# Performance work log

Measured on AMD Instinct MI355X. Metric: run time of the kernel, lower is better.

## Reference

```python
import jax, jax.numpy as jnp
import numpy as np

DIM = 2048
DIM_HEAD = 64
HEADS = 16
KV_HEADS = 2
GROUPS = HEADS // KV_HEADS  # 8
B, N = 2, 2048


def setup_inputs() -> dict:
    key = jax.random.key(0)
    k1, k2, k3, k4 = jax.random.split(key, 4)
    s = 0.02
    tokens = jax.random.normal(k1, (B, N, DIM), dtype=jnp.float32)
    context_mask = jnp.ones((B, N), dtype=bool)
    Wq = jax.random.normal(k2, (DIM, HEADS * DIM_HEAD), dtype=jnp.float32) * s
    Wkv = jax.random.normal(k3, (DIM, 2 * KV_HEADS * DIM_HEAD), dtype=jnp.float32) * s
    Wo = jax.random.normal(k4, (HEADS * DIM_HEAD, DIM), dtype=jnp.float32) * s
    return {"tokens": tokens, "context_mask": context_mask, "Wq": Wq, "Wkv": Wkv, "Wo": Wo}


def reference(tokens, context_mask, Wq, Wkv, Wo):
    b, n, _ = tokens.shape
    scale = DIM_HEAD ** -0.5
    # projections (self-attention: context = tokens)
    q = tokens @ Wq                     # [b, n, heads*dh]
    kv = tokens @ Wkv                   # [b, n, 2*kv_heads*dh]
    k, v = jnp.split(kv, 2, axis=-1)    # each [b, n, kv_heads*dh]
    # split heads: q -> [b, g, h, n, d]; k,v -> [b, h, n, d]
    q = q.reshape(b, n, GROUPS, KV_HEADS, DIM_HEAD).transpose(0, 2, 3, 1, 4)
    k = k.reshape(b, n, KV_HEADS, DIM_HEAD).transpose(0, 2, 1, 3)
    v = v.reshape(b, n, KV_HEADS, DIM_HEAD).transpose(0, 2, 1, 3)
    q = q * scale
    sim = jnp.einsum('bghid,bhjd->bghij', q, k)
    neg = -jnp.finfo(sim.dtype).max
    sim = jnp.where(context_mask[:, None, None, None, :], sim, neg)
    attn = jax.nn.softmax(sim, axis=-1)
    out = jnp.einsum('bghij,bhjd->bghid', attn, v)
    out = out.transpose(0, 3, 1, 2, 4).reshape(b, n, GROUPS * KV_HEADS * DIM_HEAD)
    return out @ Wo
```

## Files before the change

kernel.cpp:

```cpp
#include <hip/hip_runtime.h>


typedef float  f32x4   __attribute__((ext_vector_type(4)));
typedef float  f32x16  __attribute__((ext_vector_type(16)));
typedef unsigned u32x4 __attribute__((ext_vector_type(4)));
typedef __bf16 bf16x8  __attribute__((ext_vector_type(8)));
typedef __bf16 bf16x4  __attribute__((ext_vector_type(4)));

typedef f32x4  f32x4a  __attribute__((may_alias));
typedef u32x4  u32x4a  __attribute__((may_alias));
typedef bf16x8 bf16x8a __attribute__((may_alias));
typedef bf16x4 bf16x4a __attribute__((may_alias));

#define MFMA16(A, B, C) __builtin_amdgcn_mfma_f32_16x16x32_bf16(A, B, C, 0, 0, 0)
#define MFMA32(A, B, C) __builtin_amdgcn_mfma_f32_32x32x16_bf16(A, B, C, 0, 0, 0)

__device__ __forceinline__ void gload16(const void* g, void* l) {
  __builtin_amdgcn_global_load_lds(
      (const __attribute__((address_space(1))) unsigned int*)g,
      (__attribute__((address_space(3))) unsigned int*)l, 16, 0, 0);
}

__device__ __forceinline__ unsigned pack2(float a, float b) {
  union { __bf16 h[2]; unsigned u; } x;
  x.h[0] = (__bf16)a; x.h[1] = (__bf16)b;
  return x.u;
}

__device__ __forceinline__ float exp2_raw(float x) {
  float y;
  asm("v_exp_f32 %0, %1" : "=v"(y) : "v"(x));
  return y;
}

__global__ __launch_bounds__(256) void cvt_tokens(const float* __restrict__ in,
                                                  __bf16* __restrict__ out) {
  size_t idx = (size_t)blockIdx.x * 256 + threadIdx.x;
  f32x4 a = ((const f32x4a*)in)[idx * 2];
  f32x4 c = ((const f32x4a*)in)[idx * 2 + 1];
  bf16x8 v;
#pragma unroll
  for (int r = 0; r < 4; r++) { v[r] = (__bf16)a[r]; v[4 + r] = (__bf16)c[r]; }
  *(bf16x8a*)(out + idx * 8) = v;
}

__global__ __launch_bounds__(256) void transpose_all(const float* __restrict__ Wq,
                                                     const float* __restrict__ Wkv,
                                                     const float* __restrict__ Wo,
                                                     __bf16* __restrict__ WT,
                                                     __bf16* __restrict__ WoT,
                                                     float qscale) {
  const int z = blockIdx.z;
  const float* in;
  __bf16* out;
  int K, N, rowoff;
  float scale;
  if (z == 0)      { in = Wq;  out = WT;  K = 2048; N = 1024; scale = qscale; rowoff = 0; }
  else if (z == 1) { in = Wkv; out = WT;  K = 2048; N = 256;  scale = 1.f;    rowoff = 1024; }
  else             { in = Wo;  out = WoT; K = 1024; N = 2048; scale = 1.f;    rowoff = 0; }
  const int n0 = blockIdx.x * 32, k0 = blockIdx.y * 32;
  if (n0 >= N || k0 >= K) return;
  __shared__ float tile[32][33];
  const int tx = threadIdx.x, ty = threadIdx.y;
#pragma unroll
  for (int i2 = 0; i2 < 32; i2 += 8)
    tile[ty + i2][tx] = in[(size_t)(k0 + ty + i2) * N + n0 + tx];
  __syncthreads();
#pragma unroll
  for (int i2 = 0; i2 < 32; i2 += 8)
    out[(size_t)(rowoff + n0 + ty + i2) * K + k0 + tx] =
        (__bf16)(tile[tx][ty + i2] * scale);
}

__global__ __launch_bounds__(256) void build_kvpack(const __bf16* __restrict__ qkv,
                                                    __bf16* __restrict__ kv) {
  __shared__ __bf16 vt[32][64];
  const int tid = threadIdx.x;
  const int t = blockIdx.x, bh = blockIdx.y;
  const int b = bh >> 1, h = bh & 1;
  const size_t srow = (size_t)b * 2048 + (size_t)t * 32;
  __bf16* dst = kv + ((size_t)bh * 64 + t) * 4096;
  {
    int c = tid >> 5, j = tid & 31;
    bf16x8 v = *(const bf16x8a*)(qkv + (srow + j) * 1280 + 1024 + h * 64 + c * 8);
    *(bf16x8a*)(dst + tid * 8) = v;
  }
  {
    int j = tid >> 3, d8 = tid & 7;
    bf16x8 v = *(const bf16x8a*)(qkv + (srow + j) * 1280 + 1152 + h * 64 + d8 * 8);
    *(bf16x8a*)(&vt[j][d8 * 8]) = v;
  }
  __syncthreads();
  {
    int jc = tid >> 6, d = tid & 63;
    bf16x8 w;
#pragma unroll
    for (int e = 0; e < 8; e++) w[e] = vt[jc * 8 + e][d];
    *(bf16x8a*)(dst + 2048 + tid * 8) = w;
  }
}

template <int KTOT, int LDA, int LDC, bool CF32, int NX>
__global__ __launch_bounds__(512, 4) void gemm_w8(const __bf16* __restrict__ A,
                                                  const __bf16* __restrict__ Bt,
                                                  void* __restrict__ Cp) {
  __shared__ __bf16 As[2][128][64];
  __shared__ __bf16 Bs[2][64][64];
  const int tid = threadIdx.x;
  const int lane = tid & 63, wave = tid >> 6;
  const int wm = wave >> 1, wn = wave & 1;
  const int G = lane >> 4, li = lane & 15;

  const int nwg = gridDim.x;
  const int swz = (blockIdx.x & 7) * (nwg >> 3) + (blockIdx.x >> 3);
  const int m0 = (swz / NX) * 128, n0 = (swz % NX) * 64;

  const int ar0 = tid >> 3, ac0 = (tid & 7) ^ (ar0 & 7);
  const int ar1 = (512 + tid) >> 3, ac1 = (tid & 7) ^ (ar1 & 7);
  const int br = tid >> 3, bc = (tid & 7) ^ (br & 7);
  const __bf16* asrc0 = A + (size_t)(m0 + ar0) * LDA + ac0 * 8;
  const __bf16* asrc1 = A + (size_t)(m0 + ar1) * LDA + ac1 * 8;
  const __bf16* bsrc  = Bt + (size_t)(n0 + br) * KTOT + bc * 8;

  f32x4 acc[2][2] = {};
  constexpr int NSTEP = KTOT / 64;

  gload16(asrc0, &As[0][0][0] + tid * 8);
  gload16(asrc1, &As[0][0][0] + (512 + tid) * 8);
  gload16(bsrc, &Bs[0][0][0] + tid * 8);
  __syncthreads();

  for (int st = 0; st < NSTEP; ++st) {
    const int cur = st & 1;
    if (st + 1 < NSTEP) {
      const int nk = (st + 1) * 64, nb = cur ^ 1;
      gload16(asrc0 + nk, &As[nb][0][0] + tid * 8);
      gload16(asrc1 + nk, &As[nb][0][0] + (512 + tid) * 8);
      gload16(bsrc + nk, &Bs[nb][0][0] + tid * 8);
    }
    const __bf16* as = &As[cur][0][0];
    const __bf16* bs = &Bs[cur][0][0];
#pragma unroll
    for (int kk = 0; kk < 2; kk++) {
      bf16x8 af[2], bfr[2];
#pragma unroll
      for (int x = 0; x < 2; x++) {
        int r = wm * 32 + x * 16 + li;
        af[x] = *(const bf16x8a*)(as + r * 64 + (((kk * 4 + G) ^ (r & 7)) * 8));
      }
#pragma unroll
      for (int y = 0; y < 2; y++) {
        int r = wn * 32 + y * 16 + li;
        bfr[y] = *(const bf16x8a*)(bs + r * 64 + (((kk * 4 + G) ^ (r & 7)) * 8));
      }
#pragma unroll
      for (int x = 0; x < 2; x++)
#pragma unroll
        for (int y = 0; y < 2; y++)
          acc[x][y] = MFMA16(af[x], bfr[y], acc[x][y]);
    }
    __syncthreads();
  }
#pragma unroll
  for (int x = 0; x < 2; x++)
#pragma unroll
    for (int y = 0; y < 2; y++)
#pragma unroll
      for (int r = 0; r < 4; r++) {
        int row = m0 + wm * 32 + x * 16 + 4 * G + r;
        int col = n0 + wn * 32 + y * 16 + li;
        if constexpr (CF32)
          ((float*)Cp)[(size_t)row * LDC + col] = acc[x][y][r];
        else
          ((__bf16*)Cp)[(size_t)row * LDC + col] = (__bf16)acc[x][y][r];
      }
}

__global__ __launch_bounds__(512, 2) void attn_fwd(const __bf16* __restrict__ qkv,
                                                   const __bf16* __restrict__ kvpack,
                                                   __bf16* __restrict__ ao) {
  __shared__ __align__(16) char smem[81920];
  __bf16(*Qs)[64] = (__bf16(*)[64])smem;
  __bf16* kvb = (__bf16*)(smem + 32768);

  const int tid = threadIdx.x;
  const int lane = tid & 63, wave = tid >> 6;
  const int g2 = wave & 3, jh = wave >> 2;
  const int hi = lane >> 5, li = lane & 31;
  const int gt = tid & 255;
  const int qt = blockIdx.x;
  const int gh = blockIdx.y;
  const int bh = blockIdx.z;
  const int b = bh >> 1, h = bh & 1;
  const size_t row0 = (size_t)b * 2048;
  const int qrow = qt * 64;

#pragma unroll
  for (int p = 0; p < 4; p++) {
    int sl = p * 512 + tid;
    int row = sl >> 3, c = (sl & 7) ^ (row & 7);
    int head = (gh * 4 + (row >> 6)) * 2 + h;
    gload16(qkv + (row0 + qrow + (row & 63)) * 1280 + head * 64 + c * 8,
            &Qs[0][0] + sl * 8);
  }
  const __bf16* kvbase = kvpack + ((size_t)bh * 64 + jh * 32) * 4096;
  __bf16* const bufs[3] = {kvb + jh * 3 * 4096, kvb + (jh * 3 + 1) * 4096,
                           kvb + (jh * 3 + 2) * 4096};

  auto stage = [&](int t, __bf16* dst) {
    const __bf16* src = kvbase + (size_t)t * 4096;
    gload16(src + gt * 8, dst + gt * 8);
    gload16(src + (256 + gt) * 8, dst + (256 + gt) * 8);
  };

  stage(0, bufs[0]);
  stage(1, bufs[1]);
  asm volatile("s_waitcnt vmcnt(4)" ::: "memory");
  __builtin_amdgcn_s_barrier();

  const int qrA = g2 * 64 + li, qrB = g2 * 64 + 32 + li;
  u32x4 qA[4], qB[4];
#pragma unroll
  for (int dc = 0; dc < 4; dc++) {
    qA[dc] = *(const u32x4a*)(&Qs[qrA][((dc * 2 + hi) ^ (qrA & 7)) * 8]);
    qB[dc] = *(const u32x4a*)(&Qs[qrB][((dc * 2 + hi) ^ (qrB & 7)) * 8]);
    asm volatile("" : "+v"(qA[dc]), "+v"(qB[dc]));
  }

  f32x16 oA0 = {}, oA1 = {}, oB0 = {}, oB1 = {};
  asm volatile("" : "+a"(oA0), "+a"(oA1), "+a"(oB0), "+a"(oB1));
  float lA = 0.f, lB = 0.f;

  auto compute = [&](const __bf16* kb) {
    f32x16 svA = {}, svB = {};
    __builtin_amdgcn_s_setprio(1);
#pragma unroll
    for (int dc = 0; dc < 4; dc++) {
      bf16x8 kf = *(const bf16x8a*)(kb + ((dc * 2 + hi) * 32 + li) * 8);
      svA = MFMA32(kf, __builtin_bit_cast(bf16x8, qA[dc]), svA);
      svB = MFMA32(kf, __builtin_bit_cast(bf16x8, qB[dc]), svB);
    }
    __builtin_amdgcn_s_setprio(0);
#pragma unroll
    for (int i = 0; i < 16; i++) {
      svA[i] = exp2_raw(svA[i]);
      svB[i] = exp2_raw(svB[i]);
    }
    float uA[8], uB[8];
#pragma unroll
    for (int i = 0; i < 8; i++) {
      uA[i] = svA[2 * i] + svA[2 * i + 1];
      uB[i] = svB[2 * i] + svB[2 * i + 1];
    }
    lA += ((uA[0] + uA[1]) + (uA[2] + uA[3])) + ((uA[4] + uA[5]) + (uA[6] + uA[7]));
    lB += ((uB[0] + uB[1]) + (uB[2] + uB[3])) + ((uB[4] + uB[5]) + (uB[6] + uB[7]));
#pragma unroll
    for (int jc2 = 0; jc2 < 2; jc2++) {
      unsigned a0 = pack2(svA[8 * jc2 + 0], svA[8 * jc2 + 1]);
      unsigned a2 = pack2(svA[8 * jc2 + 4], svA[8 * jc2 + 5]);
      asm("v_permlane32_swap_b32 %0, %1" : "+v"(a0), "+v"(a2));
      unsigned a1 = pack2(svA[8 * jc2 + 2], svA[8 * jc2 + 3]);
      unsigned a3 = pack2(svA[8 * jc2 + 6], svA[8 * jc2 + 7]);
      asm("v_permlane32_swap_b32 %0, %1" : "+v"(a1), "+v"(a3));
      u32x4 fa = {a0, a1, a2, a3};
      bf16x8 pfA = __builtin_bit_cast(bf16x8, fa);
      unsigned b0 = pack2(svB[8 * jc2 + 0], svB[8 * jc2 + 1]);
      unsigned b2 = pack2(svB[8 * jc2 + 4], svB[8 * jc2 + 5]);
      asm("v_permlane32_swap_b32 %0, %1" : "+v"(b0), "+v"(b2));
      unsigned b1 = pack2(svB[8 * jc2 + 2], svB[8 * jc2 + 3]);
      unsigned b3 = pack2(svB[8 * jc2 + 6], svB[8 * jc2 + 7]);
      asm("v_permlane32_swap_b32 %0, %1" : "+v"(b1), "+v"(b3));
      u32x4 fb = {b0, b1, b2, b3};
      bf16x8 pfB = __builtin_bit_cast(bf16x8, fb);
      bf16x8 v0 = *(const bf16x8a*)(kb + 2048 + ((jc2 * 2 + hi) * 64 + li) * 8);
      bf16x8 v1 = *(const bf16x8a*)(kb + 2048 + ((jc2 * 2 + hi) * 64 + 32 + li) * 8);
      __builtin_amdgcn_s_setprio(1);
      oA0 = MFMA32(v0, pfA, oA0);
      oA1 = MFMA32(v1, pfA, oA1);
      oB0 = MFMA32(v0, pfB, oB0);
      oB1 = MFMA32(v1, pfB, oB1);
      __builtin_amdgcn_s_setprio(0);
    }
  };

#define ATT_TILE(T, BCUR, BNXT)                          \
  do {                                                   \
    asm volatile("s_waitcnt vmcnt(2)" ::: "memory");     \
    __builtin_amdgcn_s_barrier();                        \
    if ((T) + 2 < 32) stage((T) + 2, (BNXT));            \
    compute(BCUR);                                       \
  } while (0)

#pragma unroll 1
  for (int k = 0; k < 10; ++k) {
    int t = k * 3;
    ATT_TILE(t + 0, bufs[0], bufs[2]);
    ATT_TILE(t + 1, bufs[1], bufs[0]);
    ATT_TILE(t + 2, bufs[2], bufs[1]);
  }
  ATT_TILE(30, bufs[0], bufs[2]);
  asm volatile("s_waitcnt vmcnt(0)" ::: "memory");
  __builtin_amdgcn_s_barrier();
  compute(bufs[1]);
#undef ATT_TILE

  lA += __shfl_xor(lA, 32);
  lB += __shfl_xor(lB, 32);

  __syncthreads();
  float* mbuf = (float*)smem;
  const int slotA = (((0 * 4 + g2) * 2 + hi) * 32 + li) * 34;
  const int slotB = (((1 * 4 + g2) * 2 + hi) * 32 + li) * 34;
  if (jh == 1) {
#pragma unroll
    for (int r = 0; r < 16; r++) mbuf[slotA + r] = oA0[r];
#pragma unroll
    for (int r = 0; r < 16; r++) mbuf[slotA + 16 + r] = oA1[r];
    mbuf[slotA + 32] = lA;
#pragma unroll
    for (int r = 0; r < 16; r++) mbuf[slotB + r] = oB0[r];
#pragma unroll
    for (int r = 0; r < 16; r++) mbuf[slotB + 16 + r] = oB1[r];
    mbuf[slotB + 32] = lB;
  }
  __syncthreads();
  if (jh == 0) {
    const int head = (gh * 4 + g2) * 2 + h;
    float invA = 1.f / (lA + mbuf[slotA + 32]);
    float invB = 1.f / (lB + mbuf[slotB + 32]);
    size_t orowA = (row0 + qrow + li) * 1024 + head * 64;
    size_t orowB = (row0 + qrow + 32 + li) * 1024 + head * 64;
#pragma unroll
    for (int rb = 0; rb < 4; rb++) {
      bf16x4 wa0, wa1, wb0, wb1;
#pragma unroll
      for (int a = 0; a < 4; a++) {
        wa0[a] = (__bf16)((oA0[rb * 4 + a] + mbuf[slotA + rb * 4 + a]) * invA);
        wa1[a] = (__bf16)((oA1[rb * 4 + a] + mbuf[slotA + 16 + rb * 4 + a]) * invA);
        wb0[a] = (__bf16)((oB0[rb * 4 + a] + mbuf[slotB + rb * 4 + a]) * invB);
        wb1[a] = (__bf16)((oB1[rb * 4 + a] + mbuf[slotB + 16 + rb * 4 + a]) * invB);
      }
      *(bf16x4a*)(ao + orowA + rb * 8 + hi * 4) = wa0;
      *(bf16x4a*)(ao + orowA + 32 + rb * 8 + hi * 4) = wa1;
      *(bf16x4a*)(ao + orowB + rb * 8 + hi * 4) = wb0;
      *(bf16x4a*)(ao + orowB + 32 + rb * 8 + hi * 4) = wb1;
    }
  }
}

extern "C" void kernel_launch(void* const* d_in, const int* in_sizes, int n_in,
                              void* d_out, int out_size, void* d_ws, size_t ws_size,
                              hipStream_t stream) {
  const float* tokens = (const float*)d_in[0];
  const float* Wq  = (const float*)d_in[2];
  const float* Wkv = (const float*)d_in[3];
  const float* Wo  = (const float*)d_in[4];
  float* out = (float*)d_out;

  char* ws = (char*)d_ws;
  __bf16* Xb  = (__bf16*)(ws);
  __bf16* AO  = (__bf16*)(ws);
  __bf16* WT  = (__bf16*)(ws + 16777216);
  __bf16* WoT = (__bf16*)(ws + 22020096);
  __bf16* QKV = (__bf16*)(ws + 26214400);
  __bf16* KVp = (__bf16*)(ws + 36700160);

  const float kQScale = 0.125f * 1.44269504088896f;
  cvt_tokens<<<4096, 256, 0, stream>>>(tokens, Xb);
  transpose_all<<<dim3(64, 64, 3), dim3(32, 8), 0, stream>>>(Wq, Wkv, Wo, WT, WoT,
                                                             kQScale);
  gemm_w8<2048, 2048, 1280, false, 20><<<640, 512, 0, stream>>>(Xb, WT, QKV);
  build_kvpack<<<dim3(64, 4), 256, 0, stream>>>(QKV, KVp);
  attn_fwd<<<dim3(32, 2, 4), 512, 0, stream>>>(QKV, KVp, AO);
  gemm_w8<1024, 1024, 2048, true, 32><<<1024, 512, 0, stream>>>(AO, WoT, out);
}
```

Baseline: 126.7 us.

## Fuse KV packing into QKV GEMM epilogue, triple-buffer loads, use 32x32 MFMA

Removes the separate build_kvpack kernel. The QKV GEMM now writes its K and V tiles straight into the packed KV layout from its epilogue, and those tiles are no longer written to QKV. The GEMM mainloop moves from a double-buffered __syncthreads loop to a three-stage LDS ring with explicit vmcnt waits, and each wave uses one 32x32x16 MFMA tile instead of four 16x16 ones. This saves one launch and a global round trip, but needs more LDS per block, which may lower occupancy, and the packed writes are scattered 2-byte stores.

```diff
diff --git a/kernel.cpp b/kernel.cpp
--- a/kernel.cpp
+++ b/kernel.cpp
@@ -12,7 +12,6 @@
 typedef bf16x8 bf16x8a __attribute__((may_alias));
 typedef bf16x4 bf16x4a __attribute__((may_alias));
 
-#define MFMA16(A, B, C) __builtin_amdgcn_mfma_f32_16x16x32_bf16(A, B, C, 0, 0, 0)
 #define MFMA32(A, B, C) __builtin_amdgcn_mfma_f32_32x32x16_bf16(A, B, C, 0, 0, 0)
 
 __device__ __forceinline__ void gload16(const void* g, void* l) {
@@ -72,44 +71,17 @@
         (__bf16)(tile[tx][ty + i2] * scale);
 }
 
-__global__ __launch_bounds__(256) void build_kvpack(const __bf16* __restrict__ qkv,
-                                                    __bf16* __restrict__ kv) {
-  __shared__ __bf16 vt[32][64];
-  const int tid = threadIdx.x;
-  const int t = blockIdx.x, bh = blockIdx.y;
-  const int b = bh >> 1, h = bh & 1;
-  const size_t srow = (size_t)b * 2048 + (size_t)t * 32;
-  __bf16* dst = kv + ((size_t)bh * 64 + t) * 4096;
-  {
-    int c = tid >> 5, j = tid & 31;
-    bf16x8 v = *(const bf16x8a*)(qkv + (srow + j) * 1280 + 1024 + h * 64 + c * 8);
-    *(bf16x8a*)(dst + tid * 8) = v;
-  }
-  {
-    int j = tid >> 3, d8 = tid & 7;
-    bf16x8 v = *(const bf16x8a*)(qkv + (srow + j) * 1280 + 1152 + h * 64 + d8 * 8);
-    *(bf16x8a*)(&vt[j][d8 * 8]) = v;
-  }
-  __syncthreads();
-  {
-    int jc = tid >> 6, d = tid & 63;
-    bf16x8 w;
-#pragma unroll
-    for (int e = 0; e < 8; e++) w[e] = vt[jc * 8 + e][d];
-    *(bf16x8a*)(dst + 2048 + tid * 8) = w;
-  }
-}
-
-template <int KTOT, int LDA, int LDC, bool CF32, int NX>
+template <int KTOT, int LDA, int LDC, bool CF32, int NX, bool PACKKV>
 __global__ __launch_bounds__(512, 4) void gemm_w8(const __bf16* __restrict__ A,
                                                   const __bf16* __restrict__ Bt,
-                                                  void* __restrict__ Cp) {
-  __shared__ __bf16 As[2][128][64];
-  __shared__ __bf16 Bs[2][64][64];
+                                                  void* __restrict__ Cp,
+                                                  __bf16* __restrict__ KVp) {
+  __shared__ __bf16 As[3][128][64];
+  __shared__ __bf16 Bs[3][64][64];
   const int tid = threadIdx.x;
   const int lane = tid & 63, wave = tid >> 6;
   const int wm = wave >> 1, wn = wave & 1;
-  const int G = lane >> 4, li = lane & 15;
+  const int hi = lane >> 5, l32 = lane & 31;
 
   const int nwg = gridDim.x;
   const int swz = (blockIdx.x & 7) * (nwg >> 3) + (blockIdx.x >> 3);
@@ -122,58 +94,72 @@
   const __bf16* asrc1 = A + (size_t)(m0 + ar1) * LDA + ac1 * 8;
   const __bf16* bsrc  = Bt + (size_t)(n0 + br) * KTOT + bc * 8;
 
-  f32x4 acc[2][2] = {};
+  f32x16 acc = {};
   constexpr int NSTEP = KTOT / 64;
 
-  gload16(asrc0, &As[0][0][0] + tid * 8);
-  gload16(asrc1, &As[0][0][0] + (512 + tid) * 8);
-  gload16(bsrc, &Bs[0][0][0] + tid * 8);
-  __syncthreads();
-
-  for (int st = 0; st < NSTEP; ++st) {
-    const int cur = st & 1;
-    if (st + 1 < NSTEP) {
-      const int nk = (st + 1) * 64, nb = cur ^ 1;
+  const int rowA = wm * 32 + l32, rowB = wn * 32 + l32;
+  const int sA = rowA & 7, sB = rowB & 7;
+
+  {
+    gload16(asrc0, &As[0][0][0] + tid * 8);
+    gload16(asrc1, &As[0][0][0] + (512 + tid) * 8);
+    gload16(bsrc, &Bs[0][0][0] + tid * 8);
+    gload16(asrc0 + 64, &As[1][0][0] + tid * 8);
+    gload16(asrc1 + 64, &As[1][0][0] + (512 + tid) * 8);
+    gload16(bsrc + 64, &Bs[1][0][0] + tid * 8);
+  }
+
+#pragma unroll
+  for (int t = 0; t < NSTEP; ++t) {
+    if (t == NSTEP - 1)
+      asm volatile("s_waitcnt vmcnt(0)" ::: "memory");
+    else
+      asm volatile("s_waitcnt vmcnt(3)" ::: "memory");
+    __builtin_amdgcn_s_barrier();
+    if (t + 2 < NSTEP) {
+      const int nk = (t + 2) * 64, nb = (t + 2) % 3;
       gload16(asrc0 + nk, &As[nb][0][0] + tid * 8);
       gload16(asrc1 + nk, &As[nb][0][0] + (512 + tid) * 8);
       gload16(bsrc + nk, &Bs[nb][0][0] + tid * 8);
     }
-    const __bf16* as = &As[cur][0][0];
-    const __bf16* bs = &Bs[cur][0][0];
-#pragma unroll
-    for (int kk = 0; kk < 2; kk++) {
-      bf16x8 af[2], bfr[2];
-#pragma unroll
-      for (int x = 0; x < 2; x++) {
-        int r = wm * 32 + x * 16 + li;
-        af[x] = *(const bf16x8a*)(as + r * 64 + (((kk * 4 + G) ^ (r & 7)) * 8));
+    const __bf16* as = &As[t % 3][0][0];
+    const __bf16* bs = &Bs[t % 3][0][0];
+#pragma unroll
+    for (int ks = 0; ks < 4; ks++) {
+      bf16x8 af = *(const bf16x8a*)(as + rowA * 64 + (((ks * 2 + hi) ^ sA) * 8));
+      bf16x8 bf = *(const bf16x8a*)(bs + rowB * 64 + (((ks * 2 + hi) ^ sB) * 8));
+      acc = MFMA32(af, bf, acc);
+    }
+  }
+
+  if constexpr (PACKKV) {
+    const int ntile = swz % NX;
+    if (ntile >= 16) {
+      const int hh = ntile & 1;
+      const bool isV = ntile >= 18;
+      const int d = wn * 32 + l32;
+#pragma unroll
+      for (int r = 0; r < 16; r++) {
+        int row = m0 + wm * 32 + (r & 3) + 8 * (r >> 2) + 4 * hi;
+        int bb = row >> 11, t32 = (row & 2047) >> 5, j = row & 31;
+        __bf16* dstb = KVp + ((size_t)(bb * 2 + hh) * 64 + t32) * 4096;
+        if (isV)
+          dstb[2048 + (j >> 3) * 512 + d * 8 + (j & 7)] = (__bf16)acc[r];
+        else
+          dstb[(d >> 3) * 256 + j * 8 + (d & 7)] = (__bf16)acc[r];
       }
-#pragma unroll
-      for (int y = 0; y < 2; y++) {
-        int r = wn * 32 + y * 16 + li;
-        bfr[y] = *(const bf16x8a*)(bs + r * 64 + (((kk * 4 + G) ^ (r & 7)) * 8));
-      }
-#pragma unroll
-      for (int x = 0; x < 2; x++)
-#pragma unroll
-        for (int y = 0; y < 2; y++)
-          acc[x][y] = MFMA16(af[x], bfr[y], acc[x][y]);
-    }
-    __syncthreads();
-  }
-#pragma unroll
-  for (int x = 0; x < 2; x++)
-#pragma unroll
-    for (int y = 0; y < 2; y++)
-#pragma unroll
-      for (int r = 0; r < 4; r++) {
-        int row = m0 + wm * 32 + x * 16 + 4 * G + r;
-        int col = n0 + wn * 32 + y * 16 + li;
-        if constexpr (CF32)
-          ((float*)Cp)[(size_t)row * LDC + col] = acc[x][y][r];
-        else
-          ((__bf16*)Cp)[(size_t)row * LDC + col] = (__bf16)acc[x][y][r];
-      }
+      return;
+    }
+  }
+#pragma unroll
+  for (int r = 0; r < 16; r++) {
+    int row = m0 + wm * 32 + (r & 3) + 8 * (r >> 2) + 4 * hi;
+    int col = n0 + wn * 32 + l32;
+    if constexpr (CF32)
+      ((float*)Cp)[(size_t)row * LDC + col] = acc[r];
+    else
+      ((__bf16*)Cp)[(size_t)row * LDC + col] = (__bf16)acc[r];
+  }
 }
 
 __global__ __launch_bounds__(512, 2) void attn_fwd(const __bf16* __restrict__ qkv,
@@ -369,8 +355,9 @@
   cvt_tokens<<<4096, 256, 0, stream>>>(tokens, Xb);
   transpose_all<<<dim3(64, 64, 3), dim3(32, 8), 0, stream>>>(Wq, Wkv, Wo, WT, WoT,
                                                              kQScale);
-  gemm_w8<2048, 2048, 1280, false, 20><<<640, 512, 0, stream>>>(Xb, WT, QKV);
-  build_kvpack<<<dim3(64, 4), 256, 0, stream>>>(QKV, KVp);
+  gemm_w8<2048, 2048, 1280, false, 20, true>
+      <<<640, 512, 0, stream>>>(Xb, WT, QKV, KVp);
   attn_fwd<<<dim3(32, 2, 4), 512, 0, stream>>>(QKV, KVp, AO);
-  gemm_w8<1024, 1024, 2048, true, 32><<<1024, 512, 0, stream>>>(AO, WoT, out);
-}
+  gemm_w8<1024, 1024, 2048, true, 32, false>
+      <<<1024, 512, 0, stream>>>(AO, WoT, out, nullptr);
+}
```

Result: slower. 137.2 us (+8.3%).
